# Kernel optimization log

Hardware: AMD Instinct MI355X
Metric: run time of the kernel (lower is better)

## Reference

```python
import jax, jax.numpy as jnp
import numpy as np

Nn, Nt, Np, Ne = 100000, 30000, 400000, 1000000
IN_NODE, IN_NET, IN_PIN, IN_EDGE = 16, 8, 8, 4
H, HP, HE, L, T = 64, 16, 8, 3, 4
LOG2 = 0.6931471805599453  # ShiftedSoftplus shift


def _lrelu(x):
    return jax.nn.leaky_relu(x, 0.01)


def _ssp(x):  # DGL ShiftedSoftplus: softplus(x) - log(2)
    return jax.nn.softplus(x) - LOG2


def _forward(in_node_feat, in_net_feat, in_pin_feat, in_edge_feat,
             pins_src, pins_dst, near_src, near_dst,
             node_lin_W, node_lin_b, net_lin_W, net_lin_b,
             pin_lin_W, pin_lin_b, edge_lin_W, edge_lin_b,
             geom_W, geom_b, pins_W, pins_b,
             cf_node_W, cf_node_b, cf_e1_W, cf_e1_b, cf_e2_W, cf_e2_b,
             cf_out_W, cf_out_b, sage_pool_W, sage_pool_b,
             sage_self_W, sage_neigh_W, sage_bias,
             out1_W, out1_b, out2_W, out2_b, out3_W, out3_b,
             outn1_W, outn1_b, outn2_W, outn2_b, outn3_W, outn3_b):
    node_feat = _lrelu(in_node_feat @ node_lin_W + node_lin_b)   # [Nn,H]
    net_feat = _lrelu(in_net_feat @ net_lin_W + net_lin_b)       # [Nt,H]
    pin_feat = _lrelu(in_pin_feat @ pin_lin_W + pin_lin_b)       # [Np,HP]
    edge_feat = _lrelu(in_edge_feat @ edge_lin_W + edge_lin_b)   # [Ne,HE]

    # static degree norms for GraphConv(norm='both') on 'pins' (node->net)
    ones_p = jnp.ones((Np,), jnp.float32)
    deg_out = jax.ops.segment_sum(ones_p, pins_src, num_segments=Nn)
    deg_in = jax.ops.segment_sum(ones_p, pins_dst, num_segments=Nt)
    src_norm = jnp.clip(deg_out, 1.0, None) ** -0.5
    dst_norm = jnp.clip(deg_in, 1.0, None) ** -0.5

    for i in range(L):
        # --- 'pins' GraphConv (node -> net), norm='both' ---
        msg = (node_feat * src_norm[:, None])[pins_src]                 # [Np,H]
        agg = jax.ops.segment_sum(msg, pins_dst, num_segments=Nt)      # [Nt,H]
        net_out = (agg * dst_norm[:, None]) @ pins_W[i] + pins_b[i]

        # --- 'pinned' CFConv (net -> node), reverse pins, edge feats = pin_feat ---
        hv = net_feat @ cf_node_W[i] + cf_node_b[i]                    # [Nt,H]
        he = _ssp(pin_feat @ cf_e1_W[i] + cf_e1_b[i])
        he = _ssp(he @ cf_e2_W[i] + cf_e2_b[i])                        # [Np,H]
        m = hv[pins_dst] * he                                          # src of 'pinned' = pins_dst
        h_cf = jax.ops.segment_sum(m, pins_src, num_segments=Nn)       # dst of 'pinned' = pins_src
        node_cf = _ssp(h_cf @ cf_out_W[i] + cf_out_b[i])

        # --- 'near' SAGEConv(pool) with sigmoid edge weights ---
        ew = jax.nn.sigmoid(edge_feat @ geom_W[i] + geom_b[i])         # [Ne,1]
        hp = jax.nn.relu(node_feat @ sage_pool_W[i] + sage_pool_b[i])  # [Nn,H]
        m2 = hp[near_src] * ew                                         # [Ne,H], nonnegative
        h_neigh = jax.ops.segment_max(m2, near_dst, num_segments=Nn)
        h_neigh = jnp.maximum(h_neigh, 0.0)  # zero-degree nodes -> 0 (msgs are >= 0)
        node_sage = node_feat @ sage_self_W[i] + h_neigh @ sage_neigh_W[i] + sage_bias[i]

        # hetero max-aggregation over edge types hitting dst 'node'
        node_feat = _lrelu(jnp.maximum(node_cf, node_sage))
        net_feat = _lrelu(net_out)

    h = _lrelu(jnp.concatenate([in_node_feat, node_feat], axis=-1) @ out1_W + out1_b)
    h = _lrelu(h @ out2_W + out2_b)
    node_pred = jax.nn.sigmoid(h @ out3_W + out3_b)
    g = _lrelu(jnp.concatenate([in_net_feat, net_feat], axis=-1) @ outn1_W + outn1_b)
    g = _lrelu(g @ outn2_W + outn2_b)
    net_pred = jax.nn.sigmoid(g @ outn3_W + outn3_b)
    return node_pred, net_pred


def setup_inputs() -> dict:
    key = jax.random.key(0)
    ks = iter(jax.random.split(key, 80))

    def nrm(shape, scale=0.05):
        return jax.random.normal(next(ks), shape, jnp.float32) * scale

    inp = {}
    inp['in_node_feat'] = nrm((Nn, IN_NODE), 1.0)
    inp['in_net_feat'] = nrm((Nt, IN_NET), 1.0)
    inp['in_pin_feat'] = nrm((Np, IN_PIN), 1.0)
    inp['in_edge_feat'] = nrm((Ne, IN_EDGE), 1.0)
    inp['pins_src'] = jax.random.randint(next(ks), (Np,), 0, Nn)
    inp['pins_dst'] = jax.random.randint(next(ks), (Np,), 0, Nt)
    inp['near_src'] = jax.random.randint(next(ks), (Ne,), 0, Nn)
    inp['near_dst'] = jax.random.randint(next(ks), (Ne,), 0, Nn)
    inp['node_lin_W'] = nrm((IN_NODE, H)); inp['node_lin_b'] = nrm((H,))
    inp['net_lin_W'] = nrm((IN_NET, H)); inp['net_lin_b'] = nrm((H,))
    inp['pin_lin_W'] = nrm((IN_PIN, HP)); inp['pin_lin_b'] = nrm((HP,))
    inp['edge_lin_W'] = nrm((IN_EDGE, HE)); inp['edge_lin_b'] = nrm((HE,))
    inp['geom_W'] = nrm((L, HE, 1)); inp['geom_b'] = nrm((L, 1))
    inp['pins_W'] = nrm((L, H, H)); inp['pins_b'] = nrm((L, H))
    inp['cf_node_W'] = nrm((L, H, H)); inp['cf_node_b'] = nrm((L, H))
    inp['cf_e1_W'] = nrm((L, HP, H)); inp['cf_e1_b'] = nrm((L, H))
    inp['cf_e2_W'] = nrm((L, H, H)); inp['cf_e2_b'] = nrm((L, H))
    inp['cf_out_W'] = nrm((L, H, H)); inp['cf_out_b'] = nrm((L, H))
    inp['sage_pool_W'] = nrm((L, H, H)); inp['sage_pool_b'] = nrm((L, H))
    inp['sage_self_W'] = nrm((L, H, H))
    inp['sage_neigh_W'] = nrm((L, H, H))
    inp['sage_bias'] = nrm((L, H))
    inp['out1_W'] = nrm((IN_NODE + H, H)); inp['out1_b'] = nrm((H,))
    inp['out2_W'] = nrm((H, H)); inp['out2_b'] = nrm((H,))
    inp['out3_W'] = nrm((H, T)); inp['out3_b'] = nrm((T,))
    inp['outn1_W'] = nrm((IN_NET + H, H)); inp['outn1_b'] = nrm((H,))
    inp['outn2_W'] = nrm((H, H)); inp['outn2_b'] = nrm((H,))
    inp['outn3_W'] = nrm((H, 1)); inp['outn3_b'] = nrm((1,))
    return inp


def reference(in_node_feat, in_net_feat, in_pin_feat, in_edge_feat,
              pins_src, pins_dst, near_src, near_dst,
              node_lin_W, node_lin_b, net_lin_W, net_lin_b,
              pin_lin_W, pin_lin_b, edge_lin_W, edge_lin_b,
              geom_W, geom_b, pins_W, pins_b,
              cf_node_W, cf_node_b, cf_e1_W, cf_e1_b, cf_e2_W, cf_e2_b,
              cf_out_W, cf_out_b, sage_pool_W, sage_pool_b,
              sage_self_W, sage_neigh_W, sage_bias,
              out1_W, out1_b, out2_W, out2_b, out3_W, out3_b,
              outn1_W, outn1_b, outn2_W, outn2_b, outn3_W, outn3_b):
    return _forward(in_node_feat, in_net_feat, in_pin_feat, in_edge_feat,
                    pins_src, pins_dst, near_src, near_dst,
                    node_lin_W, node_lin_b, net_lin_W, net_lin_b,
                    pin_lin_W, pin_lin_b, edge_lin_W, edge_lin_b,
                    geom_W, geom_b, pins_W, pins_b,
                    cf_node_W, cf_node_b, cf_e1_W, cf_e1_b, cf_e2_W, cf_e2_b,
                    cf_out_W, cf_out_b, sage_pool_W, sage_pool_b,
                    sage_self_W, sage_neigh_W, sage_bias,
                    out1_W, out1_b, out2_W, out2_b, out3_W, out3_b,
                    outn1_W, outn1_b, outn2_W, outn2_b, outn3_W, outn3_b)
```

## Files before the change

kernel.cpp:

```cpp
#include <hip/hip_runtime.h>
#include <hip/hip_bf16.h>

#define DEV __device__ __forceinline__

DEV float lrelu_(float x){ return x > 0.f ? x : 0.01f * x; }
DEV float ssp_(float x){ return fmaxf(x, 0.f) + __logf(1.f + __expf(-fabsf(x))) - 0.69314718055994530942f; }
DEV float sigm_(float x){ return 1.f / (1.f + __expf(-x)); }

DEV unsigned short f2bf(float x){
    unsigned int u = __float_as_uint(x);
    unsigned int r = (u + 0x7FFFu + ((u >> 16) & 1u)) >> 16;
    return (unsigned short)r;
}
DEV float bf2f(unsigned short s){ return __uint_as_float((unsigned int)s << 16); }
DEV ushort4 pack4(float4 v){
    ushort4 u; u.x = f2bf(v.x); u.y = f2bf(v.y); u.z = f2bf(v.z); u.w = f2bf(v.w); return u;
}

DEV void fma44(float (&acc)[4][4], const float4 (&xa)[4], const float4 (&wa)[4])
{
    #pragma unroll
    for (int kk = 0; kk < 4; kk++) {
        #pragma unroll
        for (int i = 0; i < 4; i++) {
            float x = ((const float*)&xa[i])[kk];
            #pragma unroll
            for (int j = 0; j < 4; j++)
                acc[i][j] += x * ((const float*)&wa[kk])[j];
        }
    }
}

typedef short s8v __attribute__((ext_vector_type(8)));
typedef float f4v __attribute__((ext_vector_type(4)));

template<int K, int ACT, bool OUTBF>
__global__ __launch_bounds__(256) void gemm64_kernel(const float* __restrict__ X,
                                                     const float* __restrict__ W,
                                                     const float* __restrict__ B,
                                                     void* __restrict__ Yv, int nrows)
{
    constexpr int XS = K + 4;
    constexpr int KQ = K / 4;
    __shared__ float Ws[K * 64];
    __shared__ float bs[64];
    __shared__ float Xs[64 * XS];
    for (int i = threadIdx.x; i < K * 64; i += 256) Ws[i] = W[i];
    if (threadIdx.x < 64) bs[threadIdx.x] = B[threadIdx.x];
    const int tr = threadIdx.x >> 4, tc = threadIdx.x & 15;
    const int r0 = tr * 4, c0 = tc * 4;
    for (int base = blockIdx.x * 64; base < nrows; base += gridDim.x * 64) {
        __syncthreads();
        for (int i = threadIdx.x; i < 64 * KQ; i += 256) {
            int row = i / KQ, kq = (i % KQ) * 4;
            int g = base + row;
            float4 v = make_float4(0.f, 0.f, 0.f, 0.f);
            if (g < nrows) v = *(const float4*)&X[(size_t)g * K + kq];
            *(float4*)&Xs[row * XS + kq] = v;
        }
        __syncthreads();
        float acc[4][4];
        #pragma unroll
        for (int i = 0; i < 4; i++)
            #pragma unroll
            for (int j = 0; j < 4; j++) acc[i][j] = bs[c0 + j];
        #pragma unroll 4
        for (int kq = 0; kq < K; kq += 4) {
            float4 xa[4], wa[4];
            #pragma unroll
            for (int i = 0; i < 4; i++) xa[i] = *(const float4*)&Xs[(r0 + i) * XS + kq];
            #pragma unroll
            for (int j = 0; j < 4; j++) wa[j] = *(const float4*)&Ws[(kq + j) * 64 + c0];
            fma44(acc, xa, wa);
        }
        #pragma unroll
        for (int i = 0; i < 4; i++) {
            int g = base + r0 + i;
            if (g < nrows) {
                float4 o;
                float* op = (float*)&o;
                #pragma unroll
                for (int j = 0; j < 4; j++) {
                    float a = acc[i][j];
                    if (ACT == 1) a = lrelu_(a);
                    else if (ACT == 2) a = fmaxf(a, 0.f);
                    op[j] = a;
                }
                if (OUTBF) *(ushort4*)&((unsigned short*)Yv)[(size_t)g * 64 + c0] = pack4(o);
                else       *(float4*)&((float*)Yv)[(size_t)g * 64 + c0] = o;
            }
        }
    }
}

template<int ACT, bool INBF, bool OUTBF>
__global__ __launch_bounds__(256) void mfma_gemm_kernel(const void* __restrict__ Xv,
                                                        const float* __restrict__ W,
                                                        const float* __restrict__ B,
                                                        void* __restrict__ Yv, int nrows)
{
    __shared__ __align__(16) unsigned short WT[64 * 72];
    __shared__ __align__(16) unsigned short Axs[64 * 72];
    __shared__ float bs[64];
    for (int i = threadIdx.x; i < 4096; i += 256) {
        int k = i >> 6, nn = i & 63;
        WT[nn * 72 + k] = f2bf(W[i]);
    }
    if (threadIdx.x < 64) bs[threadIdx.x] = B[threadIdx.x];
    const int lane = threadIdx.x & 63, wv = threadIdx.x >> 6;
    const int l15 = lane & 15, quad = lane >> 4;
    const int arow = 16 * wv + l15;
    const int koff = quad * 8;
    for (int base = blockIdx.x * 64; base < nrows; base += gridDim.x * 64) {
        __syncthreads();
        {
            int row = threadIdx.x >> 2, kq = (threadIdx.x & 3) * 16;
            int g = base + row;
            if (INBF) {
                const unsigned short* Xb = (const unsigned short*)Xv;
                uint4 v0 = make_uint4(0,0,0,0), v1 = v0;
                if (g < nrows) {
                    v0 = *(const uint4*)&Xb[(size_t)g * 64 + kq];
                    v1 = *(const uint4*)&Xb[(size_t)g * 64 + kq + 8];
                }
                *(uint4*)&Axs[row * 72 + kq] = v0;
                *(uint4*)&Axs[row * 72 + kq + 8] = v1;
            } else {
                const float* Xf = (const float*)Xv;
                #pragma unroll
                for (int m = 0; m < 4; m++) {
                    float4 v = make_float4(0,0,0,0);
                    if (g < nrows) v = *(const float4*)&Xf[(size_t)g * 64 + kq + m * 4];
                    *(ushort4*)&Axs[row * 72 + kq + m * 4] = pack4(v);
                }
            }
        }
        __syncthreads();
        f4v acc[4];
        #pragma unroll
        for (int t = 0; t < 4; t++) acc[t] = (f4v){0.f,0.f,0.f,0.f};
        s8v a0 = *(const s8v*)&Axs[arow * 72 + koff];
        s8v a1 = *(const s8v*)&Axs[arow * 72 + 32 + koff];
        #pragma unroll
        for (int t = 0; t < 4; t++) {
            int nn = t * 16 + l15;
            s8v b0 = *(const s8v*)&WT[nn * 72 + koff];
            s8v b1 = *(const s8v*)&WT[nn * 72 + 32 + koff];
            acc[t] = __builtin_amdgcn_mfma_f32_16x16x32_bf16(a0, b0, acc[t], 0, 0, 0);
            acc[t] = __builtin_amdgcn_mfma_f32_16x16x32_bf16(a1, b1, acc[t], 0, 0, 0);
        }
        const int mrow = 16 * wv + quad * 4;
        #pragma unroll
        for (int t = 0; t < 4; t++) {
            int col = t * 16 + l15;
            float b = bs[col];
            #pragma unroll
            for (int r = 0; r < 4; r++) {
                int g = base + mrow + r;
                if (g < nrows) {
                    float a = acc[t][r] + b;
                    if (ACT == 1) a = lrelu_(a);
                    else if (ACT == 2) a = fmaxf(a, 0.f);
                    if (OUTBF) ((unsigned short*)Yv)[(size_t)g * 64 + col] = f2bf(a);
                    else       ((float*)Yv)[(size_t)g * 64 + col] = a;
                }
            }
        }
    }
}

__global__ __launch_bounds__(256) void mfma_combine_kernel(const unsigned short* __restrict__ cfb,
                                                           const unsigned short* __restrict__ nfb,
                                                           const unsigned short* __restrict__ ngb,
                                                           const float* __restrict__ Wc, const float* __restrict__ cB,
                                                           const float* __restrict__ sW, const float* __restrict__ nW,
                                                           const float* __restrict__ sB,
                                                           unsigned short* __restrict__ outb, int n)
{
    __shared__ __align__(16) unsigned short WcT[64 * 72], WsT[64 * 72], WnT[64 * 72];
    __shared__ __align__(16) unsigned short Ac[32 * 72], As[32 * 72], An[32 * 72];
    __shared__ float bc[64], bsg[64];
    for (int i = threadIdx.x; i < 4096; i += 256) {
        int k = i >> 6, nn = i & 63;
        WcT[nn * 72 + k] = f2bf(Wc[i]);
        WsT[nn * 72 + k] = f2bf(sW[i]);
        WnT[nn * 72 + k] = f2bf(nW[i]);
    }
    if (threadIdx.x < 64) { bc[threadIdx.x] = cB[threadIdx.x]; bsg[threadIdx.x] = sB[threadIdx.x]; }
    const int lane = threadIdx.x & 63, wv = threadIdx.x >> 6;
    const int l15 = lane & 15, quad = lane >> 4;
    const int arow = (wv & 1) * 16 + l15;
    const int ct0 = (wv >> 1) * 2;
    const int koff = quad * 8;
    for (int base = blockIdx.x * 32; base < n; base += gridDim.x * 32) {
        __syncthreads();
        {
            int row = threadIdx.x >> 3, kq = (threadIdx.x & 7) * 8;
            int g = base + row;
            uint4 vc = make_uint4(0,0,0,0), vf = vc, vg = vc;
            if (g < n) {
                vc = *(const uint4*)&cfb[(size_t)g * 64 + kq];
                vf = *(const uint4*)&nfb[(size_t)g * 64 + kq];
                vg = *(const uint4*)&ngb[(size_t)g * 64 + kq];
            }
            *(uint4*)&Ac[row * 72 + kq] = vc;
            *(uint4*)&As[row * 72 + kq] = vf;
            *(uint4*)&An[row * 72 + kq] = vg;
        }
        __syncthreads();
        f4v accC[2], accS[2];
        #pragma unroll
        for (int t = 0; t < 2; t++) { accC[t] = (f4v){0.f,0.f,0.f,0.f}; accS[t] = (f4v){0.f,0.f,0.f,0.f}; }
        s8v ac0 = *(const s8v*)&Ac[arow * 72 + koff];
        s8v ac1 = *(const s8v*)&Ac[arow * 72 + 32 + koff];
        s8v as0 = *(const s8v*)&As[arow * 72 + koff];
        s8v as1 = *(const s8v*)&As[arow * 72 + 32 + koff];
        s8v an0 = *(const s8v*)&An[arow * 72 + koff];
        s8v an1 = *(const s8v*)&An[arow * 72 + 32 + koff];
        #pragma unroll
        for (int t = 0; t < 2; t++) {
            int nn = (ct0 + t) * 16 + l15;
            s8v wc0 = *(const s8v*)&WcT[nn * 72 + koff];
            s8v wc1 = *(const s8v*)&WcT[nn * 72 + 32 + koff];
            accC[t] = __builtin_amdgcn_mfma_f32_16x16x32_bf16(ac0, wc0, accC[t], 0, 0, 0);
            accC[t] = __builtin_amdgcn_mfma_f32_16x16x32_bf16(ac1, wc1, accC[t], 0, 0, 0);
            s8v ws0 = *(const s8v*)&WsT[nn * 72 + koff];
            s8v ws1 = *(const s8v*)&WsT[nn * 72 + 32 + koff];
            accS[t] = __builtin_amdgcn_mfma_f32_16x16x32_bf16(as0, ws0, accS[t], 0, 0, 0);
            accS[t] = __builtin_amdgcn_mfma_f32_16x16x32_bf16(as1, ws1, accS[t], 0, 0, 0);
            s8v wn0 = *(const s8v*)&WnT[nn * 72 + koff];
            s8v wn1 = *(const s8v*)&WnT[nn * 72 + 32 + koff];
            accS[t] = __builtin_amdgcn_mfma_f32_16x16x32_bf16(an0, wn0, accS[t], 0, 0, 0);
            accS[t] = __builtin_amdgcn_mfma_f32_16x16x32_bf16(an1, wn1, accS[t], 0, 0, 0);
        }
        const int mrow = (wv & 1) * 16 + quad * 4;
        #pragma unroll
        for (int t = 0; t < 2; t++) {
            int col = (ct0 + t) * 16 + l15;
            float bcv = bc[col], bsv = bsg[col];
            #pragma unroll
            for (int r = 0; r < 4; r++) {
                int g = base + mrow + r;
                if (g < n)
                    outb[(size_t)g * 64 + col] = f2bf(lrelu_(fmaxf(ssp_(accC[t][r] + bcv), accS[t][r] + bsv)));
            }
        }
    }
}

template<int K, int C, int ACT, bool OUTBF>
__global__ __launch_bounds__(256) void lin_kernel(const float* __restrict__ X,
                                                  const float* __restrict__ W,
                                                  const float* __restrict__ B,
                                                  void* __restrict__ Yv, int nrows)
{
    constexpr int ROWS = 256 / C;
    __shared__ float Ws[K * C];
    __shared__ float bs[C];
    __shared__ float Xs[ROWS * K];
    for (int i = threadIdx.x; i < K * C; i += 256) Ws[i] = W[i];
    if (threadIdx.x < C) bs[threadIdx.x] = B[threadIdx.x];
    __syncthreads();
    const int r = threadIdx.x / C, c = threadIdx.x % C;
    for (int base = blockIdx.x * ROWS; base < nrows; base += gridDim.x * ROWS) {
        __syncthreads();
        for (int i = threadIdx.x; i < ROWS * K; i += 256) {
            int rr = base + i / K;
            Xs[i] = (rr < nrows) ? X[(size_t)rr * K + i % K] : 0.f;
        }
        __syncthreads();
        int row = base + r;
        if (row < nrows) {
            float acc = bs[c];
            #pragma unroll
            for (int k = 0; k < K; k++) acc += Xs[r * K + k] * Ws[k * C + c];
            if (ACT == 1) acc = lrelu_(acc);
            else if (ACT == 2) acc = fmaxf(acc, 0.f);
            if (OUTBF) ((unsigned short*)Yv)[(size_t)row * C + c] = f2bf(acc);
            else       ((float*)Yv)[(size_t)row * C + c] = acc;
        }
    }
}

__global__ __launch_bounds__(256) void deg_kernel(const int* __restrict__ src, const int* __restrict__ dst,
                                                  int* __restrict__ degs, int* __restrict__ degd, int np)
{
    int p = blockIdx.x * 256 + threadIdx.x;
    if (p < np) { atomicAdd(&degs[src[p]], 1); atomicAdd(&degd[dst[p]], 1); }
}

__global__ __launch_bounds__(256) void norm_kernel(int* __restrict__ arr, int n)
{
    int i = blockIdx.x * 256 + threadIdx.x;
    if (i < n) {
        int v = arr[i]; if (v < 1) v = 1;
        arr[i] = __float_as_int(rsqrtf((float)v));
    }
}

__global__ __launch_bounds__(256) void csr_count_kernel(const int* __restrict__ key, int* __restrict__ cnt, int ne)
{
    int e = blockIdx.x * 256 + threadIdx.x;
    if (e < ne) atomicAdd(&cnt[key[e]], 1);
}

__global__ __launch_bounds__(256) void scan_block_sum_kernel(const int* __restrict__ cnt, int* __restrict__ bsum, int n)
{
    __shared__ int sh[256];
    int i = blockIdx.x * 256 + threadIdx.x;
    sh[threadIdx.x] = (i < n) ? cnt[i] : 0;
    __syncthreads();
    for (int s = 128; s > 0; s >>= 1) {
        if (threadIdx.x < s) sh[threadIdx.x] += sh[threadIdx.x + s];
        __syncthreads();
    }
    if (threadIdx.x == 0) bsum[blockIdx.x] = sh[0];
}

__global__ __launch_bounds__(512) void scan_bsum_kernel(int* __restrict__ bsum, int nb, int* __restrict__ total_out)
{
    __shared__ int sh[512];
    int i = threadIdx.x;
    int v = (i < nb) ? bsum[i] : 0;
    sh[i] = v;
    __syncthreads();
    for (int s = 1; s < 512; s <<= 1) {
        int add = (i >= s) ? sh[i - s] : 0;
        __syncthreads();
        sh[i] += add;
        __syncthreads();
    }
    if (i < nb) bsum[i] = sh[i] - v;
    if (i == nb - 1) *total_out = sh[i];
}

__global__ __launch_bounds__(256) void scan_final_kernel(const int* __restrict__ cnt, const int* __restrict__ bsum,
                                                         int* __restrict__ row_start, int* __restrict__ nxt, int n)
{
    __shared__ int sh[256];
    int i = blockIdx.x * 256 + threadIdx.x;
    int v = (i < n) ? cnt[i] : 0;
    sh[threadIdx.x] = v;
    __syncthreads();
    for (int s = 1; s < 256; s <<= 1) {
        int add = (threadIdx.x >= s) ? sh[threadIdx.x - s] : 0;
        __syncthreads();
        sh[threadIdx.x] += add;
        __syncthreads();
    }
    if (i < n) {
        int excl = sh[threadIdx.x] - v + bsum[blockIdx.x];
        row_start[i] = excl;
        nxt[i] = excl;
    }
}

__global__ __launch_bounds__(256) void csr_fill_kernel(const int* __restrict__ key, int* __restrict__ nxt,
                                                       int* __restrict__ eidx, int ne, int nrows)
{
    const int color = blockIdx.x & 7;
    const int bid = blockIdx.x >> 3;
    const int nblk = gridDim.x >> 3;
    const int lo = (int)(((long long)nrows * color) >> 3);
    const int hi = (int)(((long long)nrows * (color + 1)) >> 3);
    for (int e = bid * 256 + threadIdx.x; e < ne; e += nblk * 256) {
        int k = key[e];
        if (k >= lo && k < hi) {
            int slot = atomicAdd(&nxt[k], 1);
            eidx[slot] = e;
        }
    }
}

__global__ __launch_bounds__(256) void edge_ew_kernel(const float* __restrict__ in_edge,
                                                      const float* __restrict__ elW, const float* __restrict__ elb,
                                                      const float* __restrict__ gW, const float* __restrict__ gb,
                                                      float* __restrict__ ew3, int ne)
{
    __shared__ float W[32], B[8], G[24], Gb[3];
    if (threadIdx.x < 32) W[threadIdx.x] = elW[threadIdx.x];
    if (threadIdx.x < 8)  B[threadIdx.x] = elb[threadIdx.x];
    if (threadIdx.x < 24) G[threadIdx.x] = gW[threadIdx.x];
    if (threadIdx.x < 3)  Gb[threadIdx.x] = gb[threadIdx.x];
    __syncthreads();
    for (int e = blockIdx.x * 256 + threadIdx.x; e < ne; e += gridDim.x * 256) {
        float4 x = *(const float4*)&in_edge[(size_t)e * 4];
        float ef[8];
        #pragma unroll
        for (int j = 0; j < 8; j++)
            ef[j] = lrelu_(B[j] + x.x * W[j] + x.y * W[8 + j] + x.z * W[16 + j] + x.w * W[24 + j]);
        #pragma unroll
        for (int i = 0; i < 3; i++) {
            float a = Gb[i];
            #pragma unroll
            for (int j = 0; j < 8; j++) a += ef[j] * G[i * 8 + j];
            ew3[(size_t)i * ne + e] = sigm_(a);
        }
    }
}

__global__ __launch_bounds__(256) void pins_gather_kernel(const unsigned short* __restrict__ nfb,
                                                          const float* __restrict__ snorm,
                                                          const float* __restrict__ dnorm,
                                                          const int* __restrict__ psrc,
                                                          const int* __restrict__ prow,
                                                          const int* __restrict__ peidx,
                                                          unsigned short* __restrict__ aggb, int nt)
{
    __shared__ int sS[4][64];
    __shared__ float sN[4][64];
    const int lane = threadIdx.x & 63, wv = threadIdx.x >> 6;
    for (int d = blockIdx.x * 4 + wv; d < nt; d += gridDim.x * 4) {
        int rs = prow[d], re = prow[d + 1];
        float acc = 0.f;
        for (int cbase = rs; cbase < re; cbase += 64) {
            int cnt = re - cbase; if (cnt > 64) cnt = 64;
            if (lane < cnt) {
                int p = peidx[cbase + lane];
                int s = psrc[p];
                sS[wv][lane] = s;
                sN[wv][lane] = snorm[s];
            }
            int k = 0;
            for (; k + 7 < cnt; k += 8) {
                float v[8];
                #pragma unroll
                for (int j = 0; j < 8; j++)
                    v[j] = bf2f(nfb[(size_t)sS[wv][k + j] * 64 + lane]) * sN[wv][k + j];
                acc += ((v[0] + v[1]) + (v[2] + v[3])) + ((v[4] + v[5]) + (v[6] + v[7]));
            }
            for (; k + 3 < cnt; k += 4) {
                float v0 = bf2f(nfb[(size_t)sS[wv][k]   * 64 + lane]) * sN[wv][k];
                float v1 = bf2f(nfb[(size_t)sS[wv][k+1] * 64 + lane]) * sN[wv][k+1];
                float v2 = bf2f(nfb[(size_t)sS[wv][k+2] * 64 + lane]) * sN[wv][k+2];
                float v3 = bf2f(nfb[(size_t)sS[wv][k+3] * 64 + lane]) * sN[wv][k+3];
                acc += (v0 + v1) + (v2 + v3);
            }
            for (; k < cnt; k++)
                acc += bf2f(nfb[(size_t)sS[wv][k] * 64 + lane]) * sN[wv][k];
        }
        aggb[(size_t)d * 64 + lane] = f2bf(acc * dnorm[d]);
    }
}

__global__ __launch_bounds__(256) void cf_pin6_kernel(const unsigned short* __restrict__ pinb,
                                                      const float* __restrict__ W1, const float* __restrict__ B1,
                                                      const float* __restrict__ W2, const float* __restrict__ B2,
                                                      unsigned short* __restrict__ HEb, int np)
{
    __shared__ __align__(16) unsigned short W1T[64 * 40];
    __shared__ __align__(16) unsigned short W2T[64 * 72];
    __shared__ __align__(16) unsigned short PFb[64 * 40];
    __shared__ __align__(16) unsigned short T1s[64 * 72];
    __shared__ float bs1[64], bs2[64];
    for (int i = threadIdx.x; i < 64 * 32; i += 256) {
        int n = i & 63, k = i >> 6;
        W1T[n * 40 + k] = (k < 16) ? f2bf(W1[k * 64 + n]) : (unsigned short)0;
    }
    for (int i = threadIdx.x; i < 4096; i += 256) {
        int k = i >> 6, n = i & 63;
        W2T[n * 72 + k] = f2bf(W2[i]);
    }
    if (threadIdx.x < 64) { bs1[threadIdx.x] = B1[threadIdx.x]; bs2[threadIdx.x] = B2[threadIdx.x]; }
    const int lane = threadIdx.x & 63, wv = threadIdx.x >> 6;
    const int l15 = lane & 15, quad = lane >> 4;
    const int arow = 16 * wv + l15;
    const int koff = quad * 8;
    const int mrow = 16 * wv + quad * 4;
    for (int base = blockIdx.x * 64; base < np; base += gridDim.x * 64) {
        __syncthreads();
        {
            int row = threadIdx.x >> 2, q = threadIdx.x & 3;
            int p = base + row;
            uint2 v = make_uint2(0, 0);
            if (p < np) v = *(const uint2*)&pinb[(size_t)p * 16 + q * 4];
            *(uint2*)&PFb[row * 40 + q * 4] = v;
            if (q < 2)
                *(uint4*)&PFb[row * 40 + 16 + q * 8] = make_uint4(0,0,0,0);
        }
        __syncthreads();
        {
            f4v acc1[4];
            #pragma unroll
            for (int t = 0; t < 4; t++) acc1[t] = (f4v){0.f,0.f,0.f,0.f};
            s8v a = *(const s8v*)&PFb[arow * 40 + koff];
            #pragma unroll
            for (int t = 0; t < 4; t++) {
                int n = t * 16 + l15;
                s8v b = *(const s8v*)&W1T[n * 40 + koff];
                acc1[t] = __builtin_amdgcn_mfma_f32_16x16x32_bf16(a, b, acc1[t], 0, 0, 0);
            }
            #pragma unroll
            for (int t = 0; t < 4; t++) {
                int col = t * 16 + l15;
                float b = bs1[col];
                #pragma unroll
                for (int r = 0; r < 4; r++)
                    T1s[(mrow + r) * 72 + col] = f2bf(ssp_(acc1[t][r] + b));
            }
        }
        __syncthreads();
        {
            f4v acc4[4];
            #pragma unroll
            for (int t = 0; t < 4; t++) acc4[t] = (f4v){0.f, 0.f, 0.f, 0.f};
            s8v a0 = *(const s8v*)&T1s[arow * 72 + koff];
            s8v a1 = *(const s8v*)&T1s[arow * 72 + 32 + koff];
            #pragma unroll
            for (int t = 0; t < 4; t++) {
                int n = t * 16 + l15;
                s8v b0 = *(const s8v*)&W2T[n * 72 + koff];
                s8v b1 = *(const s8v*)&W2T[n * 72 + 32 + koff];
                acc4[t] = __builtin_amdgcn_mfma_f32_16x16x32_bf16(a0, b0, acc4[t], 0, 0, 0);
                acc4[t] = __builtin_amdgcn_mfma_f32_16x16x32_bf16(a1, b1, acc4[t], 0, 0, 0);
            }
            __syncthreads();
            #pragma unroll
            for (int t = 0; t < 4; t++) {
                int col = t * 16 + l15;
                float b = bs2[col];
                #pragma unroll
                for (int r = 0; r < 4; r++)
                    T1s[(mrow + r) * 72 + col] = f2bf(ssp_(acc4[t][r] + b));
            }
        }
        __syncthreads();
        {
            int row = threadIdx.x >> 2, kq = (threadIdx.x & 3) * 16;
            int p = base + row;
            if (p < np) {
                *(uint4*)&HEb[(size_t)p * 64 + kq]     = *(const uint4*)&T1s[row * 72 + kq];
                *(uint4*)&HEb[(size_t)p * 64 + kq + 8] = *(const uint4*)&T1s[row * 72 + kq + 8];
            }
        }
    }
}

__global__ __launch_bounds__(256) void cf_gather_kernel(const unsigned short* __restrict__ HEb,
                                                        const unsigned short* __restrict__ hvb,
                                                        const int* __restrict__ pdst,
                                                        const int* __restrict__ srow,
                                                        const int* __restrict__ seidx,
                                                        unsigned short* __restrict__ cfb, int nn)
{
    __shared__ int sP[4][64], sD[4][64];
    const int lane = threadIdx.x & 63, wv = threadIdx.x >> 6;
    for (int d = blockIdx.x * 4 + wv; d < nn; d += gridDim.x * 4) {
        int rs = srow[d], re = srow[d + 1];
        float acc = 0.f;
        for (int cbase = rs; cbase < re; cbase += 64) {
            int cnt = re - cbase; if (cnt > 64) cnt = 64;
            if (lane < cnt) {
                int p = seidx[cbase + lane];
                sP[wv][lane] = p;
                sD[wv][lane] = pdst[p];
            }
            int k = 0;
            for (; k + 3 < cnt; k += 4) {
                float he[4], hv[4];
                #pragma unroll
                for (int j = 0; j < 4; j++) {
                    he[j] = bf2f(HEb[(size_t)sP[wv][k + j] * 64 + lane]);
                    hv[j] = bf2f(hvb[(size_t)sD[wv][k + j] * 64 + lane]);
                }
                acc += (he[0] * hv[0] + he[1] * hv[1]) + (he[2] * hv[2] + he[3] * hv[3]);
            }
            for (; k < cnt; k++) {
                int p0 = sP[wv][k], d0 = sD[wv][k];
                acc += bf2f(HEb[(size_t)p0 * 64 + lane]) * bf2f(hvb[(size_t)d0 * 64 + lane]);
            }
        }
        cfb[(size_t)d * 64 + lane] = f2bf(acc);
    }
}

__global__ __launch_bounds__(256) void sage_gather_kernel(const unsigned short* __restrict__ hpb,
                                                          const float* __restrict__ ew,
                                                          const int* __restrict__ esrc,
                                                          const int* __restrict__ row_start,
                                                          const int* __restrict__ eidx,
                                                          unsigned short* __restrict__ ngb, int nn)
{
    __shared__ int sS[4][64];
    __shared__ float sWt[4][64];
    const int lane = threadIdx.x & 63, wv = threadIdx.x >> 6;
    for (int d = blockIdx.x * 4 + wv; d < nn; d += gridDim.x * 4) {
        int rs = row_start[d], re = row_start[d + 1];
        float acc = 0.f;
        for (int cbase = rs; cbase < re; cbase += 64) {
            int cnt = re - cbase; if (cnt > 64) cnt = 64;
            if (lane < cnt) {
                int e = eidx[cbase + lane];
                sS[wv][lane] = esrc[e];
                sWt[wv][lane] = ew[e];
            }
            int k = 0;
            for (; k + 7 < cnt; k += 8) {
                float v[8];
                #pragma unroll
                for (int j = 0; j < 8; j++)
                    v[j] = bf2f(hpb[(size_t)sS[wv][k + j] * 64 + lane]) * sWt[wv][k + j];
                float m0 = fmaxf(fmaxf(v[0], v[1]), fmaxf(v[2], v[3]));
                float m1 = fmaxf(fmaxf(v[4], v[5]), fmaxf(v[6], v[7]));
                acc = fmaxf(acc, fmaxf(m0, m1));
            }
            for (; k + 3 < cnt; k += 4) {
                float v0 = bf2f(hpb[(size_t)sS[wv][k]   * 64 + lane]) * sWt[wv][k];
                float v1 = bf2f(hpb[(size_t)sS[wv][k+1] * 64 + lane]) * sWt[wv][k+1];
                float v2 = bf2f(hpb[(size_t)sS[wv][k+2] * 64 + lane]) * sWt[wv][k+2];
                float v3 = bf2f(hpb[(size_t)sS[wv][k+3] * 64 + lane]) * sWt[wv][k+3];
                acc = fmaxf(acc, fmaxf(fmaxf(v0, v1), fmaxf(v2, v3)));
            }
            for (; k < cnt; k++)
                acc = fmaxf(acc, bf2f(hpb[(size_t)sS[wv][k] * 64 + lane]) * sWt[wv][k]);
        }
        ngb[(size_t)d * 64 + lane] = f2bf(acc);
    }
}

__global__ __launch_bounds__(256) void node_head_mfma_kernel(const float* __restrict__ in_node,
                                                             const unsigned short* __restrict__ nfb,
                                                             const float* __restrict__ W1, const float* __restrict__ B1,
                                                             const float* __restrict__ W2, const float* __restrict__ B2,
                                                             const float* __restrict__ W3, const float* __restrict__ B3,
                                                             float* __restrict__ out, int n)
{
    __shared__ __align__(16) unsigned short W1T[64 * 104];
    __shared__ __align__(16) unsigned short W2T[64 * 72];
    __shared__ __align__(16) unsigned short W3T[16 * 72];
    __shared__ __align__(16) unsigned short Xs[64 * 104];
    __shared__ __align__(16) unsigned short H1[64 * 72];
    __shared__ float bs1[64], bs2[64], bs3[4];
    for (int i = threadIdx.x; i < 64 * 96; i += 256) {
        int k = i >> 6, nn = i & 63;
        W1T[nn * 104 + k] = (k < 80) ? f2bf(W1[k * 64 + nn]) : (unsigned short)0;
    }
    for (int i = threadIdx.x; i < 4096; i += 256) {
        int k = i >> 6, nn = i & 63;
        W2T[nn * 72 + k] = f2bf(W2[i]);
    }
    for (int i = threadIdx.x; i < 1024; i += 256) {
        int k = i >> 4, c = i & 15;
        W3T[c * 72 + k] = (c < 4) ? f2bf(W3[k * 4 + c]) : (unsigned short)0;
    }
    if (threadIdx.x < 64) { bs1[threadIdx.x] = B1[threadIdx.x]; bs2[threadIdx.x] = B2[threadIdx.x]; }
    if (threadIdx.x < 4) bs3[threadIdx.x] = B3[threadIdx.x];
    const int lane = threadIdx.x & 63, wv = threadIdx.x >> 6;
    const int l15 = lane & 15, quad = lane >> 4;
    const int arow = 16 * wv + l15;
    const int koff = quad * 8;
    const int mrow = 16 * wv + quad * 4;
    unsigned short* H2 = Xs;
    for (int base = blockIdx.x * 64; base < n; base += gridDim.x * 64) {
        __syncthreads();
        {
            int row = threadIdx.x >> 2, q = threadIdx.x & 3;
            int g = base + row;
            float4 v = make_float4(0,0,0,0);
            if (g < n) v = *(const float4*)&in_node[(size_t)g * 16 + q * 4];
            *(ushort4*)&Xs[row * 104 + q * 4] = pack4(v);
            uint4 u0 = make_uint4(0,0,0,0), u1 = u0;
            if (g < n) {
                u0 = *(const uint4*)&nfb[(size_t)g * 64 + q * 16];
                u1 = *(const uint4*)&nfb[(size_t)g * 64 + q * 16 + 8];
            }
            *(uint4*)&Xs[row * 104 + 16 + q * 16] = u0;
            *(uint4*)&Xs[row * 104 + 16 + q * 16 + 8] = u1;
            ushort4 z; z.x = 0; z.y = 0; z.z = 0; z.w = 0;
            *(ushort4*)&Xs[row * 104 + 80 + q * 4] = z;
        }
        __syncthreads();
        {
            f4v acc[4];
            #pragma unroll
            for (int t = 0; t < 4; t++) acc[t] = (f4v){0.f,0.f,0.f,0.f};
            s8v a0 = *(const s8v*)&Xs[arow * 104 + koff];
            s8v a1 = *(const s8v*)&Xs[arow * 104 + 32 + koff];
            s8v a2 = *(const s8v*)&Xs[arow * 104 + 64 + koff];
            #pragma unroll
            for (int t = 0; t < 4; t++) {
                int nn = t * 16 + l15;
                s8v b0 = *(const s8v*)&W1T[nn * 104 + koff];
                s8v b1 = *(const s8v*)&W1T[nn * 104 + 32 + koff];
                s8v b2 = *(const s8v*)&W1T[nn * 104 + 64 + koff];
                acc[t] = __builtin_amdgcn_mfma_f32_16x16x32_bf16(a0, b0, acc[t], 0, 0, 0);
                acc[t] = __builtin_amdgcn_mfma_f32_16x16x32_bf16(a1, b1, acc[t], 0, 0, 0);
                acc[t] = __builtin_amdgcn_mfma_f32_16x16x32_bf16(a2, b2, acc[t], 0, 0, 0);
            }
            #pragma unroll
            for (int t = 0; t < 4; t++) {
                int col = t * 16 + l15;
                float b = bs1[col];
                #pragma unroll
                for (int r = 0; r < 4; r++)
                    H1[(mrow + r) * 72 + col] = f2bf(lrelu_(acc[t][r] + b));
            }
        }
        __syncthreads();
        {
            f4v acc[4];
            #pragma unroll
            for (int t = 0; t < 4; t++) acc[t] = (f4v){0.f,0.f,0.f,0.f};
            s8v a0 = *(const s8v*)&H1[arow * 72 + koff];
            s8v a1 = *(const s8v*)&H1[arow * 72 + 32 + koff];
            #pragma unroll
            for (int t = 0; t < 4; t++) {
                int nn = t * 16 + l15;
                s8v b0 = *(const s8v*)&W2T[nn * 72 + koff];
                s8v b1 = *(const s8v*)&W2T[nn * 72 + 32 + koff];
                acc[t] = __builtin_amdgcn_mfma_f32_16x16x32_bf16(a0, b0, acc[t], 0, 0, 0);
                acc[t] = __builtin_amdgcn_mfma_f32_16x16x32_bf16(a1, b1, acc[t], 0, 0, 0);
            }
            __syncthreads();
            #pragma unroll
            for (int t = 0; t < 4; t++) {
                int col = t * 16 + l15;
                float b = bs2[col];
                #pragma unroll
                for (int r = 0; r < 4; r++)
                    H2[(mrow + r) * 72 + col] = f2bf(lrelu_(acc[t][r] + b));
            }
        }
        __syncthreads();
        {
            f4v acc = (f4v){0.f,0.f,0.f,0.f};
            s8v a0 = *(const s8v*)&H2[arow * 72 + koff];
            s8v a1 = *(const s8v*)&H2[arow * 72 + 32 + koff];
            s8v b0 = *(const s8v*)&W3T[l15 * 72 + koff];
            s8v b1 = *(const s8v*)&W3T[l15 * 72 + 32 + koff];
            acc = __builtin_amdgcn_mfma_f32_16x16x32_bf16(a0, b0, acc, 0, 0, 0);
            acc = __builtin_amdgcn_mfma_f32_16x16x32_bf16(a1, b1, acc, 0, 0, 0);
            if (l15 < 4) {
                float b = bs3[l15];
                #pragma unroll
                for (int r = 0; r < 4; r++) {
                    int g = base + mrow + r;
                    if (g < n) out[(size_t)g * 4 + l15] = sigm_(acc[r] + b);
                }
            }
        }
    }
}

__global__ __launch_bounds__(256) void net_head_mfma_kernel(const float* __restrict__ in_net, const float* __restrict__ tf,
                                                            const float* __restrict__ W1, const float* __restrict__ B1,
                                                            const float* __restrict__ W2, const float* __restrict__ B2,
                                                            const float* __restrict__ W3, const float* __restrict__ B3,
                                                            float* __restrict__ out, int n)
{
    __shared__ __align__(16) unsigned short W1T[64 * 104];
    __shared__ __align__(16) unsigned short W2T[64 * 72];
    __shared__ __align__(16) unsigned short W3T[16 * 72];
    __shared__ __align__(16) unsigned short Xs[64 * 104];
    __shared__ __align__(16) unsigned short H1[64 * 72];
    __shared__ float bs1[64], bs2[64], bs3[1];
    for (int i = threadIdx.x; i < 64 * 96; i += 256) {
        int k = i >> 6, nn = i & 63;
        W1T[nn * 104 + k] = (k < 72) ? f2bf(W1[k * 64 + nn]) : (unsigned short)0;
    }
    for (int i = threadIdx.x; i < 4096; i += 256) {
        int k = i >> 6, nn = i & 63;
        W2T[nn * 72 + k] = f2bf(W2[i]);
    }
    for (int i = threadIdx.x; i < 1024; i += 256) {
        int k = i >> 4, c = i & 15;
        W3T[c * 72 + k] = (c == 0) ? f2bf(W3[k]) : (unsigned short)0;
    }
    if (threadIdx.x < 64) { bs1[threadIdx.x] = B1[threadIdx.x]; bs2[threadIdx.x] = B2[threadIdx.x]; }
    if (threadIdx.x == 0) bs3[0] = B3[0];
    const int lane = threadIdx.x & 63, wv = threadIdx.x >> 6;
    const int l15 = lane & 15, quad = lane >> 4;
    const int arow = 16 * wv + l15;
    const int koff = quad * 8;
    const int mrow = 16 * wv + quad * 4;
    unsigned short* H2 = Xs;
    for (int base = blockIdx.x * 64; base < n; base += gridDim.x * 64) {
        __syncthreads();
        {
            int row = threadIdx.x >> 2, q = threadIdx.x & 3;
            int g = base + row;
            if (q < 2) {
                float4 v = make_float4(0,0,0,0);
                if (g < n) v = *(const float4*)&in_net[(size_t)g * 8 + q * 4];
                *(ushort4*)&Xs[row * 104 + q * 4] = pack4(v);
            }
            #pragma unroll
            for (int m = 0; m < 4; m++) {
                float4 v = make_float4(0,0,0,0);
                if (g < n) v = *(const float4*)&tf[(size_t)g * 64 + q * 16 + m * 4];
                *(ushort4*)&Xs[row * 104 + 8 + q * 16 + m * 4] = pack4(v);
            }
            if (q < 3) {
                ushort4 z; z.x = 0; z.y = 0; z.z = 0; z.w = 0;
                *(ushort4*)&Xs[row * 104 + 72 + q * 8] = z;
                *(ushort4*)&Xs[row * 104 + 72 + q * 8 + 4] = z;
            }
        }
        __syncthreads();
        {
            f4v acc[4];
            #pragma unroll
            for (int t = 0; t < 4; t++) acc[t] = (f4v){0.f,0.f,0.f,0.f};
            s8v a0 = *(const s8v*)&Xs[arow * 104 + koff];
            s8v a1 = *(const s8v*)&Xs[arow * 104 + 32 + koff];
            s8v a2 = *(const s8v*)&Xs[arow * 104 + 64 + koff];
            #pragma unroll
            for (int t = 0; t < 4; t++) {
                int nn = t * 16 + l15;
                s8v b0 = *(const s8v*)&W1T[nn * 104 + koff];
                s8v b1 = *(const s8v*)&W1T[nn * 104 + 32 + koff];
                s8v b2 = *(const s8v*)&W1T[nn * 104 + 64 + koff];
                acc[t] = __builtin_amdgcn_mfma_f32_16x16x32_bf16(a0, b0, acc[t], 0, 0, 0);
                acc[t] = __builtin_amdgcn_mfma_f32_16x16x32_bf16(a1, b1, acc[t], 0, 0, 0);
                acc[t] = __builtin_amdgcn_mfma_f32_16x16x32_bf16(a2, b2, acc[t], 0, 0, 0);
            }
            #pragma unroll
            for (int t = 0; t < 4; t++) {
                int col = t * 16 + l15;
                float b = bs1[col];
                #pragma unroll
                for (int r = 0; r < 4; r++)
                    H1[(mrow + r) * 72 + col] = f2bf(lrelu_(acc[t][r] + b));
            }
        }
        __syncthreads();
        {
            f4v acc[4];
            #pragma unroll
            for (int t = 0; t < 4; t++) acc[t] = (f4v){0.f,0.f,0.f,0.f};
            s8v a0 = *(const s8v*)&H1[arow * 72 + koff];
            s8v a1 = *(const s8v*)&H1[arow * 72 + 32 + koff];
            #pragma unroll
            for (int t = 0; t < 4; t++) {
                int nn = t * 16 + l15;
                s8v b0 = *(const s8v*)&W2T[nn * 72 + koff];
                s8v b1 = *(const s8v*)&W2T[nn * 72 + 32 + koff];
                acc[t] = __builtin_amdgcn_mfma_f32_16x16x32_bf16(a0, b0, acc[t], 0, 0, 0);
                acc[t] = __builtin_amdgcn_mfma_f32_16x16x32_bf16(a1, b1, acc[t], 0, 0, 0);
            }
            __syncthreads();
            #pragma unroll
            for (int t = 0; t < 4; t++) {
                int col = t * 16 + l15;
                float b = bs2[col];
                #pragma unroll
                for (int r = 0; r < 4; r++)
                    H2[(mrow + r) * 72 + col] = f2bf(lrelu_(acc[t][r] + b));
            }
        }
        __syncthreads();
        {
            f4v acc = (f4v){0.f,0.f,0.f,0.f};
            s8v a0 = *(const s8v*)&H2[arow * 72 + koff];
            s8v a1 = *(const s8v*)&H2[arow * 72 + 32 + koff];
            s8v b0 = *(const s8v*)&W3T[l15 * 72 + koff];
            s8v b1 = *(const s8v*)&W3T[l15 * 72 + 32 + koff];
            acc = __builtin_amdgcn_mfma_f32_16x16x32_bf16(a0, b0, acc, 0, 0, 0);
            acc = __builtin_amdgcn_mfma_f32_16x16x32_bf16(a1, b1, acc, 0, 0, 0);
            if (l15 == 0) {
                float b = bs3[0];
                #pragma unroll
                for (int r = 0; r < 4; r++) {
                    int g = base + mrow + r;
                    if (g < n) out[g] = sigm_(acc[r] + b);
                }
            }
        }
    }
}

extern "C" void kernel_launch(void* const* d_in, const int* in_sizes, int n_in,
                              void* d_out, int out_size, void* d_ws, size_t ws_size,
                              hipStream_t stream)
{
    (void)in_sizes; (void)n_in; (void)out_size; (void)ws_size;
    constexpr int Nn = 100000, Nt = 30000, Np = 400000, Ne = 1000000;
    constexpr int H = 64, L = 3, T = 4;

    auto fpt = [&](int i){ return (const float*)d_in[i]; };
    auto ipt = [&](int i){ return (const int*)d_in[i]; };

    const float* in_node = fpt(0);
    const float* in_net  = fpt(1);
    const float* in_pin  = fpt(2);
    const float* in_edge = fpt(3);
    const int* psrc = ipt(4);
    const int* pdst = ipt(5);
    const int* esrc = ipt(6);
    const int* edst = ipt(7);

    float* ws = (float*)d_ws;
    size_t o = 0;
    auto alloc = [&](size_t nel){ float* p = ws + o; o += nel; return p; };
    unsigned short* node_a = (unsigned short*)alloc((size_t)Nn * 32);
    unsigned short* node_b = (unsigned short*)alloc((size_t)Nn * 32);
    unsigned short* aggb   = (unsigned short*)alloc((size_t)Nt * 32);
    unsigned short* hvb    = (unsigned short*)alloc((size_t)Nt * 32);
    unsigned short* hpb    = (unsigned short*)alloc((size_t)Nn * 32);
    unsigned short* ngb    = (unsigned short*)alloc((size_t)Nn * 32);
    unsigned short* HEb    = (unsigned short*)alloc((size_t)Np * 32);
    unsigned short* cfb    = (unsigned short*)alloc((size_t)Nn * 32);
    float* net_a  = alloc((size_t)Nt * H);
    float* net_b  = alloc((size_t)Nt * H);
    unsigned short* pinb = (unsigned short*)alloc((size_t)Np * 8);
    float* ew3    = alloc((size_t)3 * Ne);
    float* snorm  = alloc((size_t)Nn);
    float* dnorm  = alloc((size_t)Nt);
    int* cnt       = (int*)alloc((size_t)Nn);
    int* row_start = (int*)alloc((size_t)Nn + 1);
    int* nxt       = (int*)alloc((size_t)Nn);
    int* eidx      = (int*)alloc((size_t)Ne);
    int* bsum      = (int*)alloc((size_t)512);
    int* pcnt      = (int*)alloc((size_t)Nt);
    int* prow      = (int*)alloc((size_t)Nt + 1);
    int* pnxt      = (int*)alloc((size_t)Nt);
    int* peidx     = (int*)alloc((size_t)Np);
    int* pbsum     = (int*)alloc((size_t)256);
    int* srow      = (int*)alloc((size_t)Nn + 1);
    int* seidx     = (int*)alloc((size_t)Np);

    constexpr int NB  = (Nn + 255) / 256;
    constexpr int NB2 = (Nt + 255) / 256;

    hipMemsetAsync(snorm, 0, (size_t)Nn * 4, stream);
    hipMemsetAsync(dnorm, 0, (size_t)Nt * 4, stream);
    deg_kernel<<<(Np + 255) / 256, 256, 0, stream>>>(psrc, pdst, (int*)snorm, (int*)dnorm, Np);
    norm_kernel<<<(Nn + 255) / 256, 256, 0, stream>>>((int*)snorm, Nn);
    norm_kernel<<<(Nt + 255) / 256, 256, 0, stream>>>((int*)dnorm, Nt);

    hipMemsetAsync(cnt, 0, (size_t)Nn * 4, stream);
    csr_count_kernel<<<(Ne + 255) / 256, 256, 0, stream>>>(edst, cnt, Ne);
    scan_block_sum_kernel<<<NB, 256, 0, stream>>>(cnt, bsum, Nn);
    scan_bsum_kernel<<<1, 512, 0, stream>>>(bsum, NB, row_start + Nn);
    scan_final_kernel<<<NB, 256, 0, stream>>>(cnt, bsum, row_start, nxt, Nn);
    csr_fill_kernel<<<2048, 256, 0, stream>>>(edst, nxt, eidx, Ne, Nn);

    hipMemsetAsync(pcnt, 0, (size_t)Nt * 4, stream);
    csr_count_kernel<<<(Np + 255) / 256, 256, 0, stream>>>(pdst, pcnt, Np);
    scan_block_sum_kernel<<<NB2, 256, 0, stream>>>(pcnt, pbsum, Nt);
    scan_bsum_kernel<<<1, 512, 0, stream>>>(pbsum, NB2, prow + Nt);
    scan_final_kernel<<<NB2, 256, 0, stream>>>(pcnt, pbsum, prow, pnxt, Nt);
    csr_fill_kernel<<<1024, 256, 0, stream>>>(pdst, pnxt, peidx, Np, Nt);

    hipMemsetAsync(cnt, 0, (size_t)Nn * 4, stream);
    csr_count_kernel<<<(Np + 255) / 256, 256, 0, stream>>>(psrc, cnt, Np);
    scan_block_sum_kernel<<<NB, 256, 0, stream>>>(cnt, bsum, Nn);
    scan_bsum_kernel<<<1, 512, 0, stream>>>(bsum, NB, srow + Nn);
    scan_final_kernel<<<NB, 256, 0, stream>>>(cnt, bsum, srow, nxt, Nn);
    csr_fill_kernel<<<1024, 256, 0, stream>>>(psrc, nxt, seidx, Np, Nn);

    gemm64_kernel<16, 1, true><<<1024, 256, 0, stream>>>(in_node, fpt(8),  fpt(9),  node_a, Nn);
    gemm64_kernel< 8, 1, false><<<469, 256, 0, stream>>>(in_net,  fpt(10), fpt(11), net_a,  Nt);
    lin_kernel<8, 16, 1, true><<<1024, 256, 0, stream>>>(in_pin, fpt(12), fpt(13), pinb, Np);
    edge_ew_kernel<<<2048, 256, 0, stream>>>(in_edge, fpt(14), fpt(15), fpt(16), fpt(17), ew3, Ne);

    unsigned short* ncur = node_a; unsigned short* nnew = node_b;
    float* tcur = net_a;  float* tnew = net_b;

    for (int i = 0; i < L; i++) {
        pins_gather_kernel<<<(Nt + 3) / 4, 256, 0, stream>>>(ncur, snorm, dnorm, psrc, prow, peidx, aggb, Nt);
        mfma_gemm_kernel<1, true, false><<<469, 256, 0, stream>>>(aggb, fpt(18) + (size_t)i * 4096, fpt(19) + (size_t)i * 64, tnew, Nt);

        mfma_gemm_kernel<0, false, true><<<469, 256, 0, stream>>>(tcur, fpt(20) + (size_t)i * 4096, fpt(21) + (size_t)i * 64, hvb, Nt);
        cf_pin6_kernel<<<1024, 256, 0, stream>>>(pinb,
                                                 fpt(22) + (size_t)i * 1024, fpt(23) + (size_t)i * 64,
                                                 fpt(24) + (size_t)i * 4096, fpt(25) + (size_t)i * 64,
                                                 HEb, Np);
        cf_gather_kernel<<<(Nn + 3) / 4, 256, 0, stream>>>(HEb, hvb, pdst, srow, seidx, cfb, Nn);

        mfma_gemm_kernel<2, true, true><<<1024, 256, 0, stream>>>(ncur, fpt(28) + (size_t)i * 4096, fpt(29) + (size_t)i * 64, hpb, Nn);
        sage_gather_kernel<<<(Nn + 3) / 4, 256, 0, stream>>>(hpb, ew3 + (size_t)i * Ne, esrc, row_start, eidx, ngb, Nn);

        mfma_combine_kernel<<<1024, 256, 0, stream>>>(cfb, ncur, ngb,
                                                      fpt(26) + (size_t)i * 4096, fpt(27) + (size_t)i * 64,
                                                      fpt(30) + (size_t)i * 4096, fpt(31) + (size_t)i * 4096,
                                                      fpt(32) + (size_t)i * 64,
                                                      nnew, Nn);

        unsigned short* t = ncur; ncur = nnew; nnew = t;
        float* tf = tcur; tcur = tnew; tnew = tf;
    }

    float* out = (float*)d_out;
    node_head_mfma_kernel<<<784, 256, 0, stream>>>(in_node, ncur, fpt(33), fpt(34), fpt(35), fpt(36), fpt(37), fpt(38), out, Nn);
    net_head_mfma_kernel<<<469, 256, 0, stream>>>(in_net, tcur, fpt(39), fpt(40), fpt(41), fpt(42), fpt(43), fpt(44), out + (size_t)Nn * T, Nt);
}
```

Measured before the change: 1.021 ms.

## Permute pin features into node-CSR order and reuse degree counts for CSR

```diff
diff --git a/kernel.cpp b/kernel.cpp
--- a/kernel.cpp
+++ b/kernel.cpp
@@ -283,18 +283,18 @@
 }
 
 __global__ __launch_bounds__(256) void deg_kernel(const int* __restrict__ src, const int* __restrict__ dst,
-                                                  int* __restrict__ degs, int* __restrict__ degd, int np)
+                                                  int* __restrict__ cnt_src, int* __restrict__ cnt_dst, int np)
 {
     int p = blockIdx.x * 256 + threadIdx.x;
-    if (p < np) { atomicAdd(&degs[src[p]], 1); atomicAdd(&degd[dst[p]], 1); }
-}
-
-__global__ __launch_bounds__(256) void norm_kernel(int* __restrict__ arr, int n)
+    if (p < np) { atomicAdd(&cnt_src[src[p]], 1); atomicAdd(&cnt_dst[dst[p]], 1); }
+}
+
+__global__ __launch_bounds__(256) void norm_out_kernel(const int* __restrict__ cnt, float* __restrict__ out, int n)
 {
     int i = blockIdx.x * 256 + threadIdx.x;
     if (i < n) {
-        int v = arr[i]; if (v < 1) v = 1;
-        arr[i] = __float_as_int(rsqrtf((float)v));
+        int v = cnt[i]; if (v < 1) v = 1;
+        out[i] = rsqrtf((float)v);
     }
 }
 
@@ -369,6 +369,20 @@
             int slot = atomicAdd(&nxt[k], 1);
             eidx[slot] = e;
         }
+    }
+}
+
+__global__ __launch_bounds__(256) void pin_permute_kernel(const int* __restrict__ seidx,
+                                                          const unsigned short* __restrict__ pinb,
+                                                          unsigned short* __restrict__ pinb_s, int np)
+{
+    int slot = blockIdx.x * 256 + threadIdx.x;
+    if (slot < np) {
+        int p = seidx[slot];
+        uint4 a = *(const uint4*)&pinb[(size_t)p * 16];
+        uint4 b = *(const uint4*)&pinb[(size_t)p * 16 + 8];
+        *(uint4*)&pinb_s[(size_t)slot * 16] = a;
+        *(uint4*)&pinb_s[(size_t)slot * 16 + 8] = b;
     }
 }
 
@@ -543,7 +557,7 @@
                                                         const int* __restrict__ seidx,
                                                         unsigned short* __restrict__ cfb, int nn)
 {
-    __shared__ int sP[4][64], sD[4][64];
+    __shared__ int sD[4][64];
     const int lane = threadIdx.x & 63, wv = threadIdx.x >> 6;
     for (int d = blockIdx.x * 4 + wv; d < nn; d += gridDim.x * 4) {
         int rs = srow[d], re = srow[d + 1];
@@ -551,23 +565,20 @@
         for (int cbase = rs; cbase < re; cbase += 64) {
             int cnt = re - cbase; if (cnt > 64) cnt = 64;
             if (lane < cnt) {
-                int p = seidx[cbase + lane];
-                sP[wv][lane] = p;
-                sD[wv][lane] = pdst[p];
+                sD[wv][lane] = pdst[seidx[cbase + lane]];
             }
             int k = 0;
             for (; k + 3 < cnt; k += 4) {
                 float he[4], hv[4];
                 #pragma unroll
                 for (int j = 0; j < 4; j++) {
-                    he[j] = bf2f(HEb[(size_t)sP[wv][k + j] * 64 + lane]);
+                    he[j] = bf2f(HEb[(size_t)(cbase + k + j) * 64 + lane]);
                     hv[j] = bf2f(hvb[(size_t)sD[wv][k + j] * 64 + lane]);
                 }
                 acc += (he[0] * hv[0] + he[1] * hv[1]) + (he[2] * hv[2] + he[3] * hv[3]);
             }
             for (; k < cnt; k++) {
-                int p0 = sP[wv][k], d0 = sD[wv][k];
-                acc += bf2f(HEb[(size_t)p0 * 64 + lane]) * bf2f(hvb[(size_t)d0 * 64 + lane]);
+                acc += bf2f(HEb[(size_t)(cbase + k) * 64 + lane]) * bf2f(hvb[(size_t)sD[wv][k] * 64 + lane]);
             }
         }
         cfb[(size_t)d * 64 + lane] = f2bf(acc);
@@ -902,11 +913,13 @@
     unsigned short* cfb    = (unsigned short*)alloc((size_t)Nn * 32);
     float* net_a  = alloc((size_t)Nt * H);
     float* net_b  = alloc((size_t)Nt * H);
-    unsigned short* pinb = (unsigned short*)alloc((size_t)Np * 8);
+    unsigned short* pinb   = (unsigned short*)alloc((size_t)Np * 8);
+    unsigned short* pinb_s = (unsigned short*)alloc((size_t)Np * 8);
     float* ew3    = alloc((size_t)3 * Ne);
     float* snorm  = alloc((size_t)Nn);
     float* dnorm  = alloc((size_t)Nt);
     int* cnt       = (int*)alloc((size_t)Nn);
+    int* ecnt      = (int*)alloc((size_t)Nn);
     int* row_start = (int*)alloc((size_t)Nn + 1);
     int* nxt       = (int*)alloc((size_t)Nn);
     int* eidx      = (int*)alloc((size_t)Ne);
@@ -922,28 +935,24 @@
     constexpr int NB  = (Nn + 255) / 256;
     constexpr int NB2 = (Nt + 255) / 256;
 
-    hipMemsetAsync(snorm, 0, (size_t)Nn * 4, stream);
-    hipMemsetAsync(dnorm, 0, (size_t)Nt * 4, stream);
-    deg_kernel<<<(Np + 255) / 256, 256, 0, stream>>>(psrc, pdst, (int*)snorm, (int*)dnorm, Np);
-    norm_kernel<<<(Nn + 255) / 256, 256, 0, stream>>>((int*)snorm, Nn);
-    norm_kernel<<<(Nt + 255) / 256, 256, 0, stream>>>((int*)dnorm, Nt);
-
     hipMemsetAsync(cnt, 0, (size_t)Nn * 4, stream);
-    csr_count_kernel<<<(Ne + 255) / 256, 256, 0, stream>>>(edst, cnt, Ne);
-    scan_block_sum_kernel<<<NB, 256, 0, stream>>>(cnt, bsum, Nn);
+    hipMemsetAsync(pcnt, 0, (size_t)Nt * 4, stream);
+    deg_kernel<<<(Np + 255) / 256, 256, 0, stream>>>(psrc, pdst, cnt, pcnt, Np);
+    norm_out_kernel<<<(Nn + 255) / 256, 256, 0, stream>>>(cnt, snorm, Nn);
+    norm_out_kernel<<<(Nt + 255) / 256, 256, 0, stream>>>(pcnt, dnorm, Nt);
+
+    hipMemsetAsync(ecnt, 0, (size_t)Nn * 4, stream);
+    csr_count_kernel<<<(Ne + 255) / 256, 256, 0, stream>>>(edst, ecnt, Ne);
+    scan_block_sum_kernel<<<NB, 256, 0, stream>>>(ecnt, bsum, Nn);
     scan_bsum_kernel<<<1, 512, 0, stream>>>(bsum, NB, row_start + Nn);
-    scan_final_kernel<<<NB, 256, 0, stream>>>(cnt, bsum, row_start, nxt, Nn);
+    scan_final_kernel<<<NB, 256, 0, stream>>>(ecnt, bsum, row_start, nxt, Nn);
     csr_fill_kernel<<<2048, 256, 0, stream>>>(edst, nxt, eidx, Ne, Nn);
 
-    hipMemsetAsync(pcnt, 0, (size_t)Nt * 4, stream);
-    csr_count_kernel<<<(Np + 255) / 256, 256, 0, stream>>>(pdst, pcnt, Np);
     scan_block_sum_kernel<<<NB2, 256, 0, stream>>>(pcnt, pbsum, Nt);
     scan_bsum_kernel<<<1, 512, 0, stream>>>(pbsum, NB2, prow + Nt);
     scan_final_kernel<<<NB2, 256, 0, stream>>>(pcnt, pbsum, prow, pnxt, Nt);
     csr_fill_kernel<<<1024, 256, 0, stream>>>(pdst, pnxt, peidx, Np, Nt);
 
-    hipMemsetAsync(cnt, 0, (size_t)Nn * 4, stream);
-    csr_count_kernel<<<(Np + 255) / 256, 256, 0, stream>>>(psrc, cnt, Np);
     scan_block_sum_kernel<<<NB, 256, 0, stream>>>(cnt, bsum, Nn);
     scan_bsum_kernel<<<1, 512, 0, stream>>>(bsum, NB, srow + Nn);
     scan_final_kernel<<<NB, 256, 0, stream>>>(cnt, bsum, srow, nxt, Nn);
@@ -954,6 +963,8 @@
     lin_kernel<8, 16, 1, true><<<1024, 256, 0, stream>>>(in_pin, fpt(12), fpt(13), pinb, Np);
     edge_ew_kernel<<<2048, 256, 0, stream>>>(in_edge, fpt(14), fpt(15), fpt(16), fpt(17), ew3, Ne);
 
+    pin_permute_kernel<<<(Np + 255) / 256, 256, 0, stream>>>(seidx, pinb, pinb_s, Np);
+
     unsigned short* ncur = node_a; unsigned short* nnew = node_b;
     float* tcur = net_a;  float* tnew = net_b;
 
@@ -962,7 +973,7 @@
         mfma_gemm_kernel<1, true, false><<<469, 256, 0, stream>>>(aggb, fpt(18) + (size_t)i * 4096, fpt(19) + (size_t)i * 64, tnew, Nt);
 
         mfma_gemm_kernel<0, false, true><<<469, 256, 0, stream>>>(tcur, fpt(20) + (size_t)i * 4096, fpt(21) + (size_t)i * 64, hvb, Nt);
-        cf_pin6_kernel<<<1024, 256, 0, stream>>>(pinb,
+        cf_pin6_kernel<<<1024, 256, 0, stream>>>(pinb_s,
                                                  fpt(22) + (size_t)i * 1024, fpt(23) + (size_t)i * 64,
                                                  fpt(24) + (size_t)i * 4096, fpt(25) + (size_t)i * 64,
                                                  HEb, Np);
```

Result: faster. 986.6 us (-3.3%).
